# Kernel tuning notes

Hardware: AMD Instinct MI355X
Metric: run time of the kernel (lower is better)

Reference implementation:

```python
import jax, jax.numpy as jnp
import numpy as np

FG_THR = 0.7
BG_THR = 0.3
NUM_PER_IMAGE = 256
NUM_POS_MAX = int(NUM_PER_IMAGE * 0.5)  # positive_ratio = 0.5
BBOX_W = (1.0, 1.0, 1.0, 1.0)
BETA = 1.0 / 9.0


def _permute(t, C):
    # N x (A*C) x H x W -> N x (H*W*A) x C, matching RPNLoss.permute
    N, _, H, W = t.shape
    t = t.reshape(N, -1, C, H, W)
    t = jnp.transpose(t, (0, 3, 4, 1, 2))
    return t.reshape(N, -1, C)


def _iou(a, b):
    # a: [N,4], b: [M,4] -> [N,M] (with +1 box convention, as in source)
    x_tl = jnp.maximum(a[:, None, 0], b[None, :, 0])
    y_tl = jnp.maximum(a[:, None, 1], b[None, :, 1])
    x_rb = jnp.minimum(a[:, None, 2], b[None, :, 2])
    y_rb = jnp.minimum(a[:, None, 3], b[None, :, 3])
    inter = jnp.clip(x_rb - x_tl + 1.0, 0.0) * jnp.clip(y_rb - y_tl + 1.0, 0.0)
    area1 = (a[:, 2] - a[:, 0] + 1.0) * (a[:, 3] - a[:, 1] + 1.0)
    area2 = (b[:, 2] - b[:, 0] + 1.0) * (b[:, 3] - b[:, 1] + 1.0)
    return inter / (area1[:, None] + area2[None, :] - inter)


def _encode(anchors, targets):
    ws = anchors[:, 2] - anchors[:, 0] + 1.0
    hs = anchors[:, 3] - anchors[:, 1] + 1.0
    x_ctr = anchors[:, 0] + 0.5 * ws
    y_ctr = anchors[:, 1] + 0.5 * hs
    t_ws = targets[:, 2] - targets[:, 0] + 1.0
    t_hs = targets[:, 3] - targets[:, 1] + 1.0
    t_x = targets[:, 0] + 0.5 * t_ws
    t_y = targets[:, 1] + 0.5 * t_hs
    wx, wy, ww, wh = BBOX_W
    tx = wx * (t_x - x_ctr) / ws
    ty = wy * (t_y - y_ctr) / hs
    tw = ww * jnp.log(t_ws / ws)
    th = wh * jnp.log(t_hs / hs)
    return jnp.stack([tx, ty, tw, th], axis=1)


def _bce_logits(l, t):
    return jnp.maximum(l, 0.0) - l * t + jnp.log1p(jnp.exp(-jnp.abs(l)))


def _per_image(anchor, logit, breg, size, target, key):
    N = anchor.shape[0]
    ious = _iou(anchor, target)  # [N, M]
    vals = ious.max(axis=1)
    ori = jnp.argmax(ious, axis=1).astype(jnp.int32)
    inds = jnp.where(vals < BG_THR, -1, ori)
    inds = jnp.where((vals >= BG_THR) & (vals < FG_THR), -2, inds)
    # low-quality matches: anchors achieving the per-target max IoU keep their argmax
    col_max = ious.max(axis=0)
    restore = (ious == col_max[None, :]).any(axis=1)
    inds = jnp.where(restore, ori, inds)
    # filter_anchors: keep anchors fully inside the image (size = (h, w))
    inside = (anchor[:, 0] >= 0) & (anchor[:, 1] >= 0) & \
             (anchor[:, 2] <= size[1] - 1.0) & (anchor[:, 3] <= size[0] - 1.0)
    inds = jnp.where(inside, inds, -2)

    pos = inds >= 0
    neg = inds == -1
    # random sampling via random priorities + fixed-size top_k with validity masks
    r = jax.random.uniform(key, (N,))
    pos_vals, pos_idx = jax.lax.top_k(jnp.where(pos, r, -1.0), NUM_POS_MAX)
    valid_pos = pos_vals >= 0.0
    num_pos = valid_pos.sum()
    neg_vals, neg_idx = jax.lax.top_k(jnp.where(neg, r, -1.0), NUM_PER_IMAGE)
    valid_neg = (neg_vals >= 0.0) & (jnp.arange(NUM_PER_IMAGE) < (NUM_PER_IMAGE - num_pos))

    # classification loss terms (BCE with logits); pos target 1, neg target 0
    vp = valid_pos.astype(logit.dtype)
    vn = valid_neg.astype(logit.dtype)
    cls_sum = jnp.sum(_bce_logits(logit[pos_idx], 1.0) * vp) + \
              jnp.sum(_bce_logits(logit[neg_idx], 0.0) * vn)
    count = num_pos + valid_neg.sum()

    m = jnp.clip(inds[pos_idx], 0, None)
    offsets = _encode(anchor[pos_idx], target[m])
    diff = jnp.abs(breg[pos_idx] - offsets)
    sl1 = jnp.where(diff < BETA, 0.5 * diff * diff / BETA, diff - 0.5 * BETA)
    reg_sum = jnp.sum(sl1 * vp[:, None])
    return cls_sum, count, reg_sum


def reference(anchors, logits, bbox_regs, sizes, targets):
    B = anchors.shape[0]
    log = _permute(logits, 1)[..., 0]      # [B, H*W*A]
    breg = _permute(bbox_regs, 4)          # [B, H*W*A, 4]
    keys = jax.random.split(jax.random.key(42), B)
    cls_s, cnt, reg_s = jax.vmap(_per_image)(anchors, log, breg, sizes, targets, keys)
    total = jnp.sum(cnt).astype(anchors.dtype)
    cls_loss = jnp.sum(cls_s) / total
    reg_loss = jnp.sum(reg_s) / total
    return jnp.stack([cls_loss, reg_loss])


def setup_inputs() -> dict:
    key = jax.random.key(0)
    ks = jax.random.split(key, 10)
    B, A, H, W, M = 4, 3, 168, 256, 32
    N = H * W * A
    IMG_H, IMG_W = 800.0, 1333.0
    x1 = jax.random.uniform(ks[0], (B, N)) * 1200.0
    y1 = jax.random.uniform(ks[1], (B, N)) * 700.0
    aw = jax.random.uniform(ks[2], (B, N)) * 300.0 + 16.0
    ah = jax.random.uniform(ks[3], (B, N)) * 300.0 + 16.0
    anchors = jnp.stack([x1, y1, x1 + aw, y1 + ah], axis=-1)  # some out of image -> filtered
    tx1 = jax.random.uniform(ks[4], (B, M)) * 1000.0
    ty1 = jax.random.uniform(ks[5], (B, M)) * 500.0
    tw = jax.random.uniform(ks[6], (B, M)) * 250.0 + 30.0
    th = jax.random.uniform(ks[7], (B, M)) * 200.0 + 30.0
    targets = jnp.stack([tx1, ty1, jnp.minimum(tx1 + tw, IMG_W - 1.0),
                         jnp.minimum(ty1 + th, IMG_H - 1.0)], axis=-1)
    logits = jax.random.normal(ks[8], (B, A, H, W), dtype=jnp.float32)
    bbox_regs = jax.random.normal(ks[9], (B, 4 * A, H, W), dtype=jnp.float32) * 0.1
    sizes = jnp.tile(jnp.array([IMG_H, IMG_W], dtype=jnp.float32), (B, 1))
    return {"anchors": anchors, "logits": logits, "bbox_regs": bbox_regs,
            "sizes": sizes, "targets": targets}
```

## Files before the change

kernel.cpp:

```cpp
#include <hip/hip_runtime.h>
#include <stdint.h>

#define RNG_MODE 1

#define Bn 4
#define An 3
#define Hn 168
#define Wn 256
#define Mn 32
#define HWn (Hn*Wn)
#define Nn (HWn*An)
#define HALFN (Nn/2)
#define POS_CAP 8192
#define BND_CAP 2048
#define NPERIM 256
#define NPOSMAX 128
#define FG_THR 0.7f
#define BG_THR 0.3f
#define BETA (1.0f/9.0f)

#define OFF_KEYS   0
#define OFF_COLMAX 8
#define OFF_POSCNT 136
#define OFF_BNDCNT 140
#define OFF_BOUND  144
#define OFF_NEED   148
#define OFF_COUNT  152
#define OFF_CLS    153
#define OFF_REG    154
#define OFF_HIST   160
#define ZERO_BEG   8
#define ZERO_END   4256
#define OFF_CAT    4256
#define OFF_M      520352
#define OFF_PLIST  1036448
#define OFF_BLIST  1101984

__device__ __forceinline__ uint32_t rotl32(uint32_t v, int n) { return (v << n) | (v >> (32 - n)); }

__device__ __forceinline__ void tf2x32(uint32_t k0, uint32_t k1, uint32_t x0, uint32_t x1,
                                       uint32_t& o0, uint32_t& o1) {
    uint32_t k2 = k0 ^ k1 ^ 0x1BD11BDAu;
    x0 += k0; x1 += k1;
    x0 += x1; x1 = rotl32(x1, 13); x1 ^= x0;
    x0 += x1; x1 = rotl32(x1, 15); x1 ^= x0;
    x0 += x1; x1 = rotl32(x1, 26); x1 ^= x0;
    x0 += x1; x1 = rotl32(x1, 6);  x1 ^= x0;
    x0 += k1; x1 += k2 + 1u;
    x0 += x1; x1 = rotl32(x1, 17); x1 ^= x0;
    x0 += x1; x1 = rotl32(x1, 29); x1 ^= x0;
    x0 += x1; x1 = rotl32(x1, 16); x1 ^= x0;
    x0 += x1; x1 = rotl32(x1, 24); x1 ^= x0;
    x0 += k2; x1 += k0 + 2u;
    x0 += x1; x1 = rotl32(x1, 13); x1 ^= x0;
    x0 += x1; x1 = rotl32(x1, 15); x1 ^= x0;
    x0 += x1; x1 = rotl32(x1, 26); x1 ^= x0;
    x0 += x1; x1 = rotl32(x1, 6);  x1 ^= x0;
    x0 += k0; x1 += k1 + 3u;
    x0 += x1; x1 = rotl32(x1, 17); x1 ^= x0;
    x0 += x1; x1 = rotl32(x1, 29); x1 ^= x0;
    x0 += x1; x1 = rotl32(x1, 16); x1 ^= x0;
    x0 += x1; x1 = rotl32(x1, 24); x1 ^= x0;
    x0 += k1; x1 += k2 + 4u;
    x0 += x1; x1 = rotl32(x1, 13); x1 ^= x0;
    x0 += x1; x1 = rotl32(x1, 15); x1 ^= x0;
    x0 += x1; x1 = rotl32(x1, 26); x1 ^= x0;
    x0 += x1; x1 = rotl32(x1, 6);  x1 ^= x0;
    x0 += k2; x1 += k0 + 5u;
    o0 = x0; o1 = x1;
}

__device__ __forceinline__ uint32_t rng_m23(uint32_t k0, uint32_t k1, uint32_t i) {
    uint32_t o0, o1;
    tf2x32(k0, k1, 0u, i, o0, o1);
    return (o0 ^ o1) >> 9;
}

__device__ __forceinline__ float iou_one(float a0, float a1, float a2, float a3,
                                         float t0, float t1, float t2, float t3) {
    float xtl = fmaxf(a0, t0), ytl = fmaxf(a1, t1);
    float xrb = fminf(a2, t2), yrb = fminf(a3, t3);
    float iw = fmaxf(xrb - xtl + 1.0f, 0.0f);
    float ih = fmaxf(yrb - ytl + 1.0f, 0.0f);
    float inter = iw * ih;
    float area1 = (a2 - a0 + 1.0f) * (a3 - a1 + 1.0f);
    float area2 = (t2 - t0 + 1.0f) * (t3 - t1 + 1.0f);
    return inter / (area1 + area2 - inter);
}

__global__ void k0_init(uint32_t* __restrict__ ws) {
    int t = blockIdx.x * blockDim.x + threadIdx.x;
    for (int j = ZERO_BEG + t; j < ZERO_END; j += gridDim.x * blockDim.x) ws[j] = 0u;
    if (t == 0) {
        for (int b = 0; b < Bn; ++b) {
            uint32_t o0, o1;
            tf2x32(0u, 42u, 0u, (uint32_t)b, o0, o1);
            ws[OFF_KEYS + 2*b] = o0; ws[OFF_KEYS + 2*b + 1] = o1;
        }
    }
}

#define K1_BLOCKS 64
__global__ void __launch_bounds__(256) k1_colmax(const float* __restrict__ anchors,
                                                 const float* __restrict__ targets,
                                                 uint32_t* __restrict__ ws) {
    int b = blockIdx.y;
    __shared__ float tg[Mn * 4];
    __shared__ float part[4][Mn];
    if (threadIdx.x < Mn * 4) tg[threadIdx.x] = targets[b * Mn * 4 + threadIdx.x];
    __syncthreads();
    float cm[Mn];
    #pragma unroll
    for (int t = 0; t < Mn; ++t) cm[t] = 0.0f;
    const int stride = K1_BLOCKS * 256;
    for (int i = blockIdx.x * 256 + threadIdx.x; i < Nn; i += stride) {
        float4 av = ((const float4*)anchors)[b * Nn + i];
        #pragma unroll
        for (int t = 0; t < Mn; ++t) {
            float iou = iou_one(av.x, av.y, av.z, av.w, tg[t*4], tg[t*4+1], tg[t*4+2], tg[t*4+3]);
            cm[t] = fmaxf(cm[t], iou);
        }
    }
    #pragma unroll
    for (int t = 0; t < Mn; ++t) {
        #pragma unroll
        for (int o = 32; o > 0; o >>= 1) cm[t] = fmaxf(cm[t], __shfl_xor(cm[t], o, 64));
    }
    int wid = threadIdx.x >> 6, lane = threadIdx.x & 63;
    if (lane == 0) {
        #pragma unroll
        for (int t = 0; t < Mn; ++t) part[wid][t] = cm[t];
    }
    __syncthreads();
    if (threadIdx.x < Mn) {
        float v = fmaxf(fmaxf(part[0][threadIdx.x], part[1][threadIdx.x]),
                        fmaxf(part[2][threadIdx.x], part[3][threadIdx.x]));
        atomicMax(&ws[OFF_COLMAX + b * Mn + threadIdx.x], __float_as_uint(v));
    }
}

__global__ void __launch_bounds__(256) k2_cat(const float* __restrict__ anchors,
                                              const float* __restrict__ targets,
                                              const float* __restrict__ sizes,
                                              uint32_t* __restrict__ ws) {
    int b = blockIdx.y;
    int i = blockIdx.x * 256 + threadIdx.x;
    __shared__ float tg[Mn * 4];
    __shared__ float cmf[Mn];
    if (threadIdx.x < Mn * 4) tg[threadIdx.x] = targets[b * Mn * 4 + threadIdx.x];
    if (threadIdx.x < Mn) cmf[threadIdx.x] = __uint_as_float(ws[OFF_COLMAX + b * Mn + threadIdx.x]);
    __syncthreads();
    float4 av = ((const float4*)anchors)[b * Nn + i];
    float rowmax = -1.0f; int ori = 0; bool restore = false;
    for (int t = 0; t < Mn; ++t) {
        float iou = iou_one(av.x, av.y, av.z, av.w, tg[t*4], tg[t*4+1], tg[t*4+2], tg[t*4+3]);
        if (iou > rowmax) { rowmax = iou; ori = t; }
        restore = restore || (iou == cmf[t]);
    }
    float sh = sizes[b * 2 + 0], sw = sizes[b * 2 + 1];
    bool inside = (av.x >= 0.0f) && (av.y >= 0.0f) && (av.z <= sw - 1.0f) && (av.w <= sh - 1.0f);
    int cat = 0;
    if (inside) {
        if (restore || rowmax >= FG_THR) cat = 2;
        else if (rowmax < BG_THR) cat = 1;
    }
    uint32_t k0 = ws[OFF_KEYS + 2 * b], k1 = ws[OFF_KEYS + 2 * b + 1];
    uint32_t m = rng_m23(k0, k1, (uint32_t)i);
    ws[OFF_CAT + b * Nn + i] = (uint32_t)cat;
    ws[OFF_M + b * Nn + i] = m;
    if (cat == 2) {
        uint32_t p = atomicAdd(&ws[OFF_POSCNT + b], 1u);
        if (p < POS_CAP) {
            ws[OFF_PLIST + ((uint32_t)b * POS_CAP + p) * 2 + 0] = m;
            ws[OFF_PLIST + ((uint32_t)b * POS_CAP + p) * 2 + 1] = (uint32_t)i | ((uint32_t)ori << 17);
        }
    } else if (cat == 1) {
        atomicAdd(&ws[OFF_HIST + b * 1024 + (m >> 13)], 1u);
    }
}

__global__ void k25_bound(uint32_t* __restrict__ ws) {
    int b = blockIdx.x;
    if (threadIdx.x != 0) return;
    uint32_t pc = ws[OFF_POSCNT + b];
    int num_pos = (pc < (uint32_t)NPOSMAX) ? (int)pc : NPOSMAX;
    int k_neg = NPERIM - num_pos;
    int cum = 0, boundary = -1, needed = 0;
    for (int bk = 1023; bk >= 0; --bk) {
        int c = (int)ws[OFF_HIST + b * 1024 + bk];
        if (cum + c >= k_neg) { boundary = bk; needed = k_neg - cum; break; }
        cum += c;
    }
    int neg_sel = (boundary >= 0) ? k_neg : cum;
    ws[OFF_BOUND + b] = (uint32_t)boundary;
    ws[OFF_NEED + b] = (uint32_t)needed;
    atomicAdd(&ws[OFF_COUNT], (uint32_t)(num_pos + neg_sel));
}

__global__ void __launch_bounds__(256) k3_neg(const float* __restrict__ logits,
                                              uint32_t* __restrict__ ws) {
    int b = blockIdx.y;
    int i = blockIdx.x * 256 + threadIdx.x;
    float local = 0.0f;
    uint32_t cat = ws[OFF_CAT + b * Nn + i];
    if (cat == 1u) {
        uint32_t m = ws[OFF_M + b * Nn + i];
        int bk = (int)(m >> 13);
        int bd = (int)(int32_t)ws[OFF_BOUND + b];
        if (bk > bd) {
            int a = i % An, hw = i / An;
            float l = logits[(b * An + a) * HWn + hw];
            local = fmaxf(l, 0.0f) + log1pf(expf(-fabsf(l)));
        } else if (bk == bd) {
            uint32_t p = atomicAdd(&ws[OFF_BNDCNT + b], 1u);
            if (p < BND_CAP) {
                ws[OFF_BLIST + ((uint32_t)b * BND_CAP + p) * 2 + 0] = m;
                ws[OFF_BLIST + ((uint32_t)b * BND_CAP + p) * 2 + 1] = (uint32_t)i;
            }
        }
    }
    __shared__ float red[256];
    red[threadIdx.x] = local;
    __syncthreads();
    for (int s = 128; s > 0; s >>= 1) {
        if ((int)threadIdx.x < s) red[threadIdx.x] += red[threadIdx.x + s];
        __syncthreads();
    }
    if (threadIdx.x == 0 && red[0] != 0.0f) atomicAdd((float*)&ws[OFF_CLS], red[0]);
}

__device__ __forceinline__ bool sel_less(uint2 a, uint2 b) {
    return (a.x > b.x) || (a.x == b.x && a.y < b.y);
}

__device__ void bitonic_sort_shared(uint2* buf, int n) {
    for (int k = 2; k <= n; k <<= 1) {
        for (int j = k >> 1; j > 0; j >>= 1) {
            for (int t = (int)threadIdx.x; t < n; t += 256) {
                int ixj = t ^ j;
                if (ixj > t) {
                    uint2 x = buf[t], y = buf[ixj];
                    bool up = ((t & k) == 0);
                    bool sw = up ? sel_less(y, x) : sel_less(x, y);
                    if (sw) { buf[t] = y; buf[ixj] = x; }
                }
            }
            __syncthreads();
        }
    }
}

__global__ void __launch_bounds__(256) k4_final(const float* __restrict__ anchors,
                                                const float* __restrict__ targets,
                                                const float* __restrict__ logits,
                                                const float* __restrict__ bregs,
                                                uint32_t* __restrict__ ws) {
    int b = blockIdx.x;
    __shared__ uint2 buf[BND_CAP];
    __shared__ float red[256];
    float cls = 0.0f, reg = 0.0f;

    uint32_t pcu = ws[OFF_POSCNT + b];
    int pc = (pcu < (uint32_t)POS_CAP) ? (int)pcu : POS_CAP;
    const uint32_t* plist = ws + OFF_PLIST + (size_t)b * POS_CAP * 2;
    int psel = (pc < NPOSMAX) ? pc : NPOSMAX;
    bool use_buf = false;
    if (pc > NPOSMAX) {
        int n = (pc < BND_CAP) ? pc : BND_CAP;
        for (int j = (int)threadIdx.x; j < n; j += 256) buf[j] = make_uint2(plist[2*j], plist[2*j+1]);
        int npad = 1; while (npad < n) npad <<= 1;
        for (int j = (int)threadIdx.x; j < npad; j += 256) if (j >= n) buf[j] = make_uint2(0u, 0xFFFFFFFFu);
        __syncthreads();
        bitonic_sort_shared(buf, npad);
        use_buf = true;
        psel = (NPOSMAX < n) ? NPOSMAX : n;
    }
    for (int j = (int)threadIdx.x; j < psel; j += 256) {
        uint32_t packed = use_buf ? buf[j].y : plist[2*j+1];
        int i = (int)(packed & 0x1FFFFu);
        int ori = (int)(packed >> 17);
        int a = i % An, hw = i / An;
        float l = logits[(b * An + a) * HWn + hw];
        cls += fmaxf(l, 0.0f) - l + log1pf(expf(-fabsf(l)));
        float4 av = ((const float4*)anchors)[b * Nn + i];
        float4 tv = ((const float4*)targets)[b * Mn + ori];
        float aws = av.z - av.x + 1.0f, ahs = av.w - av.y + 1.0f;
        float axc = av.x + 0.5f * aws, ayc = av.y + 0.5f * ahs;
        float tws = tv.z - tv.x + 1.0f, ths = tv.w - tv.y + 1.0f;
        float txc = tv.x + 0.5f * tws, tyc = tv.y + 0.5f * ths;
        float off0 = (txc - axc) / aws;
        float off1 = (tyc - ayc) / ahs;
        float off2 = logf(tws / aws);
        float off3 = logf(ths / ahs);
        float br0 = bregs[(b * 12 + a * 4 + 0) * HWn + hw];
        float br1 = bregs[(b * 12 + a * 4 + 1) * HWn + hw];
        float br2 = bregs[(b * 12 + a * 4 + 2) * HWn + hw];
        float br3 = bregs[(b * 12 + a * 4 + 3) * HWn + hw];
        float d;
        d = fabsf(br0 - off0); reg += (d < BETA) ? 0.5f * d * d / BETA : d - 0.5f * BETA;
        d = fabsf(br1 - off1); reg += (d < BETA) ? 0.5f * d * d / BETA : d - 0.5f * BETA;
        d = fabsf(br2 - off2); reg += (d < BETA) ? 0.5f * d * d / BETA : d - 0.5f * BETA;
        d = fabsf(br3 - off3); reg += (d < BETA) ? 0.5f * d * d / BETA : d - 0.5f * BETA;
    }
    __syncthreads();

    int need = (int)ws[OFF_NEED + b];
    if (need > 0) {
        uint32_t nbu = ws[OFF_BNDCNT + b];
        int nb = (nbu < (uint32_t)BND_CAP) ? (int)nbu : BND_CAP;
        const uint32_t* blist = ws + OFF_BLIST + (size_t)b * BND_CAP * 2;
        for (int j = (int)threadIdx.x; j < nb; j += 256) buf[j] = make_uint2(blist[2*j], blist[2*j+1]);
        int npad = 1; while (npad < nb) npad <<= 1;
        for (int j = (int)threadIdx.x; j < npad; j += 256) if (j >= nb) buf[j] = make_uint2(0u, 0xFFFFFFFFu);
        __syncthreads();
        bitonic_sort_shared(buf, npad);
        int sel = (need < nb) ? need : nb;
        for (int j = (int)threadIdx.x; j < sel; j += 256) {
            int i = (int)buf[j].y;
            int a = i % An, hw = i / An;
            float l = logits[(b * An + a) * HWn + hw];
            cls += fmaxf(l, 0.0f) + log1pf(expf(-fabsf(l)));
        }
    }

    red[threadIdx.x] = cls;
    __syncthreads();
    for (int s = 128; s > 0; s >>= 1) {
        if ((int)threadIdx.x < s) red[threadIdx.x] += red[threadIdx.x + s];
        __syncthreads();
    }
    if (threadIdx.x == 0 && red[0] != 0.0f) atomicAdd((float*)&ws[OFF_CLS], red[0]);
    __syncthreads();
    red[threadIdx.x] = reg;
    __syncthreads();
    for (int s = 128; s > 0; s >>= 1) {
        if ((int)threadIdx.x < s) red[threadIdx.x] += red[threadIdx.x + s];
        __syncthreads();
    }
    if (threadIdx.x == 0 && red[0] != 0.0f) atomicAdd((float*)&ws[OFF_REG], red[0]);
}

__global__ void k5_out(const uint32_t* __restrict__ ws, float* __restrict__ out) {
    if (blockIdx.x == 0 && threadIdx.x == 0) {
        float cnt = (float)ws[OFF_COUNT];
        out[0] = __uint_as_float(ws[OFF_CLS]) / cnt;
        out[1] = __uint_as_float(ws[OFF_REG]) / cnt;
    }
}

extern "C" void kernel_launch(void* const* d_in, const int* in_sizes, int n_in,
                              void* d_out, int out_size, void* d_ws, size_t ws_size,
                              hipStream_t stream) {
    const float* anchors = (const float*)d_in[0];
    const float* logits  = (const float*)d_in[1];
    const float* bregs   = (const float*)d_in[2];
    const float* sizes   = (const float*)d_in[3];
    const float* targets = (const float*)d_in[4];
    float* out = (float*)d_out;
    uint32_t* ws = (uint32_t*)d_ws;

    dim3 gridN(Nn / 256, Bn);
    k0_init<<<dim3(64), dim3(256), 0, stream>>>(ws);
    k1_colmax<<<dim3(K1_BLOCKS, Bn), dim3(256), 0, stream>>>(anchors, targets, ws);
    k2_cat<<<gridN, dim3(256), 0, stream>>>(anchors, targets, sizes, ws);
    k25_bound<<<dim3(Bn), dim3(64), 0, stream>>>(ws);
    k3_neg<<<gridN, dim3(256), 0, stream>>>(logits, ws);
    k4_final<<<dim3(Bn), dim3(256), 0, stream>>>(anchors, targets, logits, bregs, ws);
    k5_out<<<dim3(1), dim3(64), 0, stream>>>(ws, out);
}
```

Before: 186.1 us.

## Pack cat/rand into one word, widen colmax grid, parallel-scan bound, fuse output

Stores category and random mantissa in a single packed word, which halves workspace traffic between the categorisation and negative-loss kernels. The column-max kernel now uses 256 blocks with two anchors per thread and reads targets directly instead of staging them in shared memory. The bucket-boundary search becomes a 256-thread suffix scan in place of a serial single-thread loop. The final output kernel is folded into k4 through a last-block-done atomic counter, which removes one launch at the cost of a threadfence and extra atomics.

```diff
diff --git a/kernel.cpp b/kernel.cpp
--- a/kernel.cpp
+++ b/kernel.cpp
@@ -1,7 +1,5 @@
 #include <hip/hip_runtime.h>
 #include <stdint.h>
-
-#define RNG_MODE 1
 
 #define Bn 4
 #define An 3
@@ -10,7 +8,6 @@
 #define Mn 32
 #define HWn (Hn*Wn)
 #define Nn (HWn*An)
-#define HALFN (Nn/2)
 #define POS_CAP 8192
 #define BND_CAP 2048
 #define NPERIM 256
@@ -28,13 +25,13 @@
 #define OFF_COUNT  152
 #define OFF_CLS    153
 #define OFF_REG    154
+#define OFF_DONE   155
 #define OFF_HIST   160
 #define ZERO_BEG   8
 #define ZERO_END   4256
-#define OFF_CAT    4256
-#define OFF_M      520352
-#define OFF_PLIST  1036448
-#define OFF_BLIST  1101984
+#define OFF_PACK   4256
+#define OFF_PLIST  520352
+#define OFF_BLIST  585888
 
 __device__ __forceinline__ uint32_t rotl32(uint32_t v, int n) { return (v << n) | (v >> (32 - n)); }
 
@@ -100,26 +97,24 @@
     }
 }
 
-#define K1_BLOCKS 64
+#define K1_BLOCKS 256
 __global__ void __launch_bounds__(256) k1_colmax(const float* __restrict__ anchors,
                                                  const float* __restrict__ targets,
                                                  uint32_t* __restrict__ ws) {
     int b = blockIdx.y;
-    __shared__ float tg[Mn * 4];
     __shared__ float part[4][Mn];
-    if (threadIdx.x < Mn * 4) tg[threadIdx.x] = targets[b * Mn * 4 + threadIdx.x];
-    __syncthreads();
+    int i1 = blockIdx.x * 256 + threadIdx.x;
+    int i2 = i1 + K1_BLOCKS * 256;
+    bool v2 = (i2 < Nn);
+    float4 a1 = ((const float4*)anchors)[b * Nn + i1];
+    float4 a2 = ((const float4*)anchors)[b * Nn + (v2 ? i2 : i1)];
     float cm[Mn];
-    #pragma unroll
-    for (int t = 0; t < Mn; ++t) cm[t] = 0.0f;
-    const int stride = K1_BLOCKS * 256;
-    for (int i = blockIdx.x * 256 + threadIdx.x; i < Nn; i += stride) {
-        float4 av = ((const float4*)anchors)[b * Nn + i];
-        #pragma unroll
-        for (int t = 0; t < Mn; ++t) {
-            float iou = iou_one(av.x, av.y, av.z, av.w, tg[t*4], tg[t*4+1], tg[t*4+2], tg[t*4+3]);
-            cm[t] = fmaxf(cm[t], iou);
-        }
+    #pragma unroll 8
+    for (int t = 0; t < Mn; ++t) {
+        float4 tv = ((const float4*)targets)[b * Mn + t];
+        float u1 = iou_one(a1.x, a1.y, a1.z, a1.w, tv.x, tv.y, tv.z, tv.w);
+        float u2 = iou_one(a2.x, a2.y, a2.z, a2.w, tv.x, tv.y, tv.z, tv.w);
+        cm[t] = fmaxf(u1, v2 ? u2 : 0.0f);
     }
     #pragma unroll
     for (int t = 0; t < Mn; ++t) {
@@ -145,77 +140,103 @@
                                               uint32_t* __restrict__ ws) {
     int b = blockIdx.y;
     int i = blockIdx.x * 256 + threadIdx.x;
-    __shared__ float tg[Mn * 4];
-    __shared__ float cmf[Mn];
-    if (threadIdx.x < Mn * 4) tg[threadIdx.x] = targets[b * Mn * 4 + threadIdx.x];
-    if (threadIdx.x < Mn) cmf[threadIdx.x] = __uint_as_float(ws[OFF_COLMAX + b * Mn + threadIdx.x]);
-    __syncthreads();
     float4 av = ((const float4*)anchors)[b * Nn + i];
     float rowmax = -1.0f; int ori = 0; bool restore = false;
+    #pragma unroll 8
     for (int t = 0; t < Mn; ++t) {
-        float iou = iou_one(av.x, av.y, av.z, av.w, tg[t*4], tg[t*4+1], tg[t*4+2], tg[t*4+3]);
+        float4 tv = ((const float4*)targets)[b * Mn + t];
+        float cmf = __uint_as_float(ws[OFF_COLMAX + b * Mn + t]);
+        float iou = iou_one(av.x, av.y, av.z, av.w, tv.x, tv.y, tv.z, tv.w);
         if (iou > rowmax) { rowmax = iou; ori = t; }
-        restore = restore || (iou == cmf[t]);
+        restore = restore || (iou == cmf);
     }
     float sh = sizes[b * 2 + 0], sw = sizes[b * 2 + 1];
     bool inside = (av.x >= 0.0f) && (av.y >= 0.0f) && (av.z <= sw - 1.0f) && (av.w <= sh - 1.0f);
-    int cat = 0;
+    uint32_t cat = 0;
     if (inside) {
         if (restore || rowmax >= FG_THR) cat = 2;
         else if (rowmax < BG_THR) cat = 1;
     }
     uint32_t k0 = ws[OFF_KEYS + 2 * b], k1 = ws[OFF_KEYS + 2 * b + 1];
     uint32_t m = rng_m23(k0, k1, (uint32_t)i);
-    ws[OFF_CAT + b * Nn + i] = (uint32_t)cat;
-    ws[OFF_M + b * Nn + i] = m;
-    if (cat == 2) {
+    ws[OFF_PACK + b * Nn + i] = m | (cat << 24);
+    if (cat == 2u) {
         uint32_t p = atomicAdd(&ws[OFF_POSCNT + b], 1u);
         if (p < POS_CAP) {
             ws[OFF_PLIST + ((uint32_t)b * POS_CAP + p) * 2 + 0] = m;
             ws[OFF_PLIST + ((uint32_t)b * POS_CAP + p) * 2 + 1] = (uint32_t)i | ((uint32_t)ori << 17);
         }
-    } else if (cat == 1) {
+    } else if (cat == 1u) {
         atomicAdd(&ws[OFF_HIST + b * 1024 + (m >> 13)], 1u);
     }
 }
 
-__global__ void k25_bound(uint32_t* __restrict__ ws) {
+__global__ void __launch_bounds__(256) k25_bound(uint32_t* __restrict__ ws) {
     int b = blockIdx.x;
-    if (threadIdx.x != 0) return;
+    int t = threadIdx.x;
+    __shared__ uint32_t csum[256];
+    uint32_t h[4];
+    uint32_t sum = 0;
+    #pragma unroll
+    for (int j = 0; j < 4; ++j) { h[j] = ws[OFF_HIST + b * 1024 + 4 * t + j]; sum += h[j]; }
+    csum[t] = sum;
+    __syncthreads();
+    for (int off = 1; off < 256; off <<= 1) {
+        uint32_t mine = csum[t];
+        uint32_t add = (t + off < 256) ? csum[t + off] : 0u;
+        __syncthreads();
+        csum[t] = mine + add;
+        __syncthreads();
+    }
     uint32_t pc = ws[OFF_POSCNT + b];
     int num_pos = (pc < (uint32_t)NPOSMAX) ? (int)pc : NPOSMAX;
     int k_neg = NPERIM - num_pos;
-    int cum = 0, boundary = -1, needed = 0;
-    for (int bk = 1023; bk >= 0; --bk) {
-        int c = (int)ws[OFF_HIST + b * 1024 + bk];
-        if (cum + c >= k_neg) { boundary = bk; needed = k_neg - cum; break; }
-        cum += c;
-    }
-    int neg_sel = (boundary >= 0) ? k_neg : cum;
-    ws[OFF_BOUND + b] = (uint32_t)boundary;
-    ws[OFF_NEED + b] = (uint32_t)needed;
-    atomicAdd(&ws[OFF_COUNT], (uint32_t)(num_pos + neg_sel));
+    uint32_t total = csum[0];
+    if ((int)total < k_neg) {
+        if (t == 0) {
+            ws[OFF_BOUND + b] = 0xFFFFFFFFu;
+            ws[OFF_NEED + b] = 0u;
+            atomicAdd(&ws[OFF_COUNT], (uint32_t)(num_pos + (int)total));
+        }
+        return;
+    }
+    uint32_t incl = csum[t];
+    uint32_t next = (t < 255) ? csum[t + 1] : 0u;
+    if ((int)incl >= k_neg && (int)next < k_neg) {
+        int cum = (int)next;
+        int boundary = -1, needed = 0;
+        #pragma unroll
+        for (int j = 3; j >= 0; --j) {
+            int c = (int)h[j];
+            if (cum + c >= k_neg) { boundary = 4 * t + j; needed = k_neg - cum; break; }
+            cum += c;
+        }
+        ws[OFF_BOUND + b] = (uint32_t)boundary;
+        ws[OFF_NEED + b] = (uint32_t)needed;
+        atomicAdd(&ws[OFF_COUNT], (uint32_t)(num_pos + k_neg));
+    }
 }
 
 __global__ void __launch_bounds__(256) k3_neg(const float* __restrict__ logits,
                                               uint32_t* __restrict__ ws) {
     int b = blockIdx.y;
     int i = blockIdx.x * 256 + threadIdx.x;
+    int bd = (int)(int32_t)ws[OFF_BOUND + b];
+    uint32_t p = ws[OFF_PACK + b * Nn + i];
+    uint32_t cat = p >> 24;
     float local = 0.0f;
-    uint32_t cat = ws[OFF_CAT + b * Nn + i];
     if (cat == 1u) {
-        uint32_t m = ws[OFF_M + b * Nn + i];
+        uint32_t m = p & 0x7FFFFFu;
         int bk = (int)(m >> 13);
-        int bd = (int)(int32_t)ws[OFF_BOUND + b];
         if (bk > bd) {
             int a = i % An, hw = i / An;
             float l = logits[(b * An + a) * HWn + hw];
             local = fmaxf(l, 0.0f) + log1pf(expf(-fabsf(l)));
         } else if (bk == bd) {
-            uint32_t p = atomicAdd(&ws[OFF_BNDCNT + b], 1u);
-            if (p < BND_CAP) {
-                ws[OFF_BLIST + ((uint32_t)b * BND_CAP + p) * 2 + 0] = m;
-                ws[OFF_BLIST + ((uint32_t)b * BND_CAP + p) * 2 + 1] = (uint32_t)i;
+            uint32_t q = atomicAdd(&ws[OFF_BNDCNT + b], 1u);
+            if (q < BND_CAP) {
+                ws[OFF_BLIST + ((uint32_t)b * BND_CAP + q) * 2 + 0] = m;
+                ws[OFF_BLIST + ((uint32_t)b * BND_CAP + q) * 2 + 1] = (uint32_t)i;
             }
         }
     }
@@ -254,7 +275,8 @@
                                                 const float* __restrict__ targets,
                                                 const float* __restrict__ logits,
                                                 const float* __restrict__ bregs,
-                                                uint32_t* __restrict__ ws) {
+                                                uint32_t* __restrict__ ws,
+                                                float* __restrict__ out) {
     int b = blockIdx.x;
     __shared__ uint2 buf[BND_CAP];
     __shared__ float red[256];
@@ -337,14 +359,17 @@
         if ((int)threadIdx.x < s) red[threadIdx.x] += red[threadIdx.x + s];
         __syncthreads();
     }
-    if (threadIdx.x == 0 && red[0] != 0.0f) atomicAdd((float*)&ws[OFF_REG], red[0]);
-}
-
-__global__ void k5_out(const uint32_t* __restrict__ ws, float* __restrict__ out) {
-    if (blockIdx.x == 0 && threadIdx.x == 0) {
-        float cnt = (float)ws[OFF_COUNT];
-        out[0] = __uint_as_float(ws[OFF_CLS]) / cnt;
-        out[1] = __uint_as_float(ws[OFF_REG]) / cnt;
+    if (threadIdx.x == 0) {
+        if (red[0] != 0.0f) atomicAdd((float*)&ws[OFF_REG], red[0]);
+        __threadfence();
+        uint32_t old = atomicAdd(&ws[OFF_DONE], 1u);
+        if (old == Bn - 1) {
+            float cls_tot = __uint_as_float(atomicAdd(&ws[OFF_CLS], 0u));
+            float reg_tot = __uint_as_float(atomicAdd(&ws[OFF_REG], 0u));
+            float cnt = (float)atomicAdd(&ws[OFF_COUNT], 0u);
+            out[0] = cls_tot / cnt;
+            out[1] = reg_tot / cnt;
+        }
     }
 }
 
@@ -363,8 +388,7 @@
     k0_init<<<dim3(64), dim3(256), 0, stream>>>(ws);
     k1_colmax<<<dim3(K1_BLOCKS, Bn), dim3(256), 0, stream>>>(anchors, targets, ws);
     k2_cat<<<gridN, dim3(256), 0, stream>>>(anchors, targets, sizes, ws);
-    k25_bound<<<dim3(Bn), dim3(64), 0, stream>>>(ws);
+    k25_bound<<<dim3(Bn), dim3(256), 0, stream>>>(ws);
     k3_neg<<<gridN, dim3(256), 0, stream>>>(logits, ws);
-    k4_final<<<dim3(Bn), dim3(256), 0, stream>>>(anchors, targets, logits, bregs, ws);
-    k5_out<<<dim3(1), dim3(64), 0, stream>>>(ws, out);
-}
+    k4_final<<<dim3(Bn), dim3(256), 0, stream>>>(anchors, targets, logits, bregs, ws, out);
+}
```

Result: faster. 177.7 us (-4.5%).
